# Kernel optimization log

Measured on AMD Instinct MI355X. Metric: run time of the kernel, lower is better.

The kernel has to match this reference:

```python
import jax, jax.numpy as jnp
from jax import lax
import numpy as np

EPS = 1e-12      # F.normalize eps
TOP_N = 250      # top negatives selected
SMOOTH = 1e-5    # soft dice smooth


def _dilate10(m):
    # == 10 iterations of 3x3x3 binary max-pool dilation. m: [B,D,H,W] float.
    for _ in range(10):
        m = lax.reduce_window(m, 0.0, lax.max, (1, 3, 3, 3), (1, 1, 1, 1), 'SAME')
    return m


def _self_loss(feature, lab):
    # feature: [B,C,D,H,W], lab: [B,D,H,W] int
    feat = jnp.moveaxis(feature, 1, -1)                       # [B,D,H,W,C]
    pos = (lab == 1)
    posf = pos.astype(feat.dtype)
    cnt = posf.sum()
    std = (feat * posf[..., None]).sum((0, 1, 2, 3)) / jnp.maximum(cnt, 1.0)
    std = jnp.where(cnt > 0, std, 0.0)                        # [C]
    std_n = std / jnp.maximum(jnp.linalg.norm(std), EPS)
    feat_n = feat / jnp.maximum(jnp.linalg.norm(feat, axis=-1, keepdims=True), EPS)
    # cosine similarity of per-voxel normalized features vs normalized mean positive
    sim = jnp.einsum('bdhwc,c->bdhw', feat_n, std_n)

    # positive term: mean over positives of (1 - sim)
    pos_loss = jnp.where(cnt > 0, ((1.0 - sim) * posf).sum() / jnp.maximum(cnt, 1.0), 0.0)

    # easily-misclassified ring: dilate(pos,10) & ~pos; mean relu(sim)
    mis = (_dilate10(posf) > 0) & (~pos)
    misf = mis.astype(sim.dtype)
    mcnt = misf.sum()
    mis_loss = jnp.where(mcnt > 0, (jax.nn.relu(sim) * misf).sum() / jnp.maximum(mcnt, 1.0), 0.0)

    # hard negatives: top-250 sims among label==0, scatter to mask, dilate, & ~pos
    neg = (lab == 0)
    neg_sims = jnp.where(neg, sim, -jnp.inf).reshape(-1)
    top_vals, top_idx = lax.top_k(neg_sims, TOP_N)
    hsm = jnp.zeros(neg_sims.shape[0], sim.dtype).at[top_idx].set(
        jnp.where(jnp.isfinite(top_vals), 1.0, 0.0)).reshape(sim.shape)
    fin = (_dilate10(hsm) > 0) & (~pos)
    finf = fin.astype(sim.dtype)
    fcnt = finf.sum()
    neg_loss = jnp.where(fcnt > 0, (jax.nn.relu(sim) * finf).sum() / jnp.maximum(fcnt, 1.0), 0.0)

    return pos_loss + mis_loss + neg_loss


def _ce_dice(net_output, target):
    lab = target[:, 0]                                        # [B,D,H,W]
    logp = jax.nn.log_softmax(net_output, axis=1)
    ce = -jnp.mean(jnp.take_along_axis(logp, target, axis=1))
    probs = jnp.exp(logp)                                     # softmax_helper_dim1
    nc = net_output.shape[1]
    onehot = jax.nn.one_hot(lab, nc, axis=1, dtype=probs.dtype)  # [B,nc,D,H,W]
    axes = (0, 2, 3, 4)                                       # batch_dice=True
    tp = (probs * onehot).sum(axes)
    fp = (probs * (1.0 - onehot)).sum(axes)
    fn = ((1.0 - probs) * onehot).sum(axes)
    dc = (2.0 * tp + SMOOTH) / (2.0 * tp + fp + fn + SMOOTH + 1e-8)
    dice = -jnp.mean(dc[1:])                                  # do_bg=False
    return ce, dice


def reference(feature, net_output, target):
    ce, dice = _ce_dice(net_output, target)
    sl = _self_loss(feature, target[:, 0])
    return 1.0 * ce + 1.0 * dice + 5.0 * sl


def setup_inputs():
    key = jax.random.key(0)
    k1, k2, k3 = jax.random.split(key, 3)
    B, C, D, H, W = 2, 32, 64, 128, 128
    NC = 2
    feature = jax.random.normal(k1, (B, C, D, H, W), jnp.float32)
    net_output = jax.random.normal(k2, (B, NC, D, H, W), jnp.float32)
    target = jax.random.randint(k3, (B, 1, D, H, W), 0, 2).astype(jnp.int32)
    return {'feature': feature, 'net_output': net_output, 'target': target}
```

## Files before the change

### kernel.cpp

```cpp
#include <hip/hip_runtime.h>
#include <stdint.h>

typedef unsigned int u32;
typedef unsigned long long u64;

#define BB 2
#define CC 32
#define DD 64
#define HH 128
#define WW 128
#define SS (DD*HH*WW)
#define NN (BB*SS)
#define NQ (NN/4)
#define NWORDS (NN/64)
#define EPSF 1e-12f
#define TOPN 250u

struct Ctrl {
  u32 done4, tie, pad0, pad1;
};

struct Acc {
  double ce, tp, fp, fn;
  double stdsum[CC];
  double pos_num, mis_num, fin_num;
  u64 cnt, mcnt, fcnt;
};

__device__ __forceinline__ float waveRedF(float v){
#pragma unroll
  for (int o = 32; o; o >>= 1) v += __shfl_xor(v, o);
  return v;
}
__device__ __forceinline__ u32 waveRedU(u32 v){
#pragma unroll
  for (int o = 32; o; o >>= 1) v += __shfl_xor(v, o);
  return v;
}
__device__ __forceinline__ void red_d(double* dst, float v, volatile float* sh){
  int lane = threadIdx.x & 63, wid = threadIdx.x >> 6;
  v = waveRedF(v);
  if (lane == 0) sh[wid] = v;
  __syncthreads();
  if (threadIdx.x == 0){
    float t = 0.f;
    for (int i = 0; i < (int)(blockDim.x >> 6); i++) t += sh[i];
    atomicAdd(dst, (double)t);
  }
  __syncthreads();
}
__device__ __forceinline__ void red_u(u64* dst, u32 v, volatile u32* sh){
  int lane = threadIdx.x & 63, wid = threadIdx.x >> 6;
  v = waveRedU(v);
  if (lane == 0) sh[wid] = v;
  __syncthreads();
  if (threadIdx.x == 0){
    u32 t = 0;
    for (int i = 0; i < (int)(blockDim.x >> 6); i++) t += sh[i];
    atomicAdd(dst, (u64)t);
  }
  __syncthreads();
}

__device__ __forceinline__ u32 sortkey(float f){
  u32 u = __float_as_uint(f);
  return (u & 0x80000000u) ? ~u : (u | 0x80000000u);
}

__device__ __forceinline__ void select_top(const u32* __restrict__ hist, u32 nbins,
                                           u32 k, u32* shres, u32* binOut, u32* kremOut){
  __syncthreads();
  if (threadIdx.x < 64){
    int lane = threadIdx.x;
    u32 running = 0; bool found = false;
    for (u32 chunk = 0; chunk * 64 < nbins && !found; chunk++){
      int bin = (int)nbins - 1 - (int)(chunk * 64 + (u32)lane);
      u32 val = (bin >= 0) ? hist[bin] : 0u;
      u32 p = val;
#pragma unroll
      for (int o = 1; o < 64; o <<= 1){ u32 t = __shfl_up(p, o); if (lane >= o) p += t; }
      u32 tot = __shfl(p, 63);
      u32 incl = running + p, excl = incl - val;
      bool hit = (excl < k) && (incl >= k);
      u64 mb = __ballot(hit);
      if (mb){
        int hl = __ffsll((unsigned long long)mb) - 1;
        if (lane == hl){ shres[0] = (u32)bin; shres[1] = k - excl; }
        found = true;
      } else running += tot;
    }
    if (!found && lane == 0){ shres[0] = 0; shres[1] = k; }
  }
  __syncthreads();
  *binOut = shres[0]; *kremOut = shres[1];
}

__global__ __launch_bounds__(256) void k_ce(const float* __restrict__ net,
                                            const int* __restrict__ tgt,
                                            u64* __restrict__ pbits, Acc* acc){
  __shared__ u32 nibsh[256];
  __shared__ float shf[4]; __shared__ u32 shu[4];
  float ce = 0.f, tp = 0.f, fp = 0.f, fnn = 0.f;
  u32 cnt = 0;
  const u32 stride = 1024u * 256u;
#pragma unroll 1
  for (u32 it = 0; it < 2; it++){
    u32 q = blockIdx.x * 256u + threadIdx.x + it * stride;
    u32 v = q * 4u;
    u32 b = v >> 20, s = v & (SS - 1);
    int4 l4 = *(const int4*)(tgt + v);
    u32 nib = (l4.x ? 1u : 0u) | (l4.y ? 2u : 0u) | (l4.z ? 4u : 0u) | (l4.w ? 8u : 0u);
    cnt += __popc(nib);
    __syncthreads();
    nibsh[threadIdx.x] = nib;
    {
      const float* nb = net + (size_t)(b * 2) * SS + s;
      float4 x0 = *(const float4*)(nb);
      float4 x1 = *(const float4*)(nb + SS);
      float xs0[4] = {x0.x, x0.y, x0.z, x0.w};
      float xs1[4] = {x1.x, x1.y, x1.z, x1.w};
#pragma unroll
      for (int j = 0; j < 4; j++){
        int lab = (nib >> j) & 1;
        float m = fmaxf(xs0[j], xs1[j]);
        float lse = m + logf(expf(xs0[j] - m) + expf(xs1[j] - m));
        ce += lse - (lab ? xs1[j] : xs0[j]);
        float p1 = expf(xs1[j] - lse);
        if (lab){ tp += p1; fnn += 1.0f - p1; } else fp += p1;
      }
    }
    __syncthreads();
    if (threadIdx.x < 16){
      u64 o = 0;
#pragma unroll
      for (int j = 0; j < 16; j++)
        o |= (u64)(nibsh[threadIdx.x * 16 + j] & 0xFu) << (4 * j);
      pbits[blockIdx.x * 16u + it * 16384u + threadIdx.x] = o;
    }
  }
  red_d(&acc->ce, ce, shf);
  red_d(&acc->tp, tp, shf);
  red_d(&acc->fp, fp, shf);
  red_d(&acc->fn, fnn, shf);
  red_u(&acc->cnt, cnt, shu);
}

__global__ __launch_bounds__(256) void k_std(const float* __restrict__ feat,
                                             const u64* __restrict__ pbits, Acc* acc){
  u32 c = blockIdx.x & 31u;
  u32 chunk = blockIdx.x >> 5;
  u32 vbase = chunk * 65536u;
  u32 b = vbase >> 20;
  u32 s0 = vbase & (SS - 1);
  const float* fp = feat + (size_t)b * CC * SS + (size_t)c * SS + s0;
  const u64* pb = pbits + (vbase >> 6);
  float a = 0.f;
#pragma unroll 8
  for (u32 i = 0; i < 64; i++){
    u32 off = i * 1024u + threadIdx.x * 4u;
    float4 f = *(const float4*)(fp + off);
    u32 bits = (u32)(pb[off >> 6] >> (off & 63u)) & 0xFu;
    if (bits & 1u) a += f.x;
    if (bits & 2u) a += f.y;
    if (bits & 4u) a += f.z;
    if (bits & 8u) a += f.w;
  }
  __shared__ float sh[4];
  int lane = threadIdx.x & 63, wid = threadIdx.x >> 6;
  a = waveRedF(a);
  if (lane == 0) sh[wid] = a;
  __syncthreads();
  if (threadIdx.x == 0)
    atomicAdd(&acc->stdsum[c], (double)(sh[0] + sh[1] + sh[2] + sh[3]));
}

__global__ __launch_bounds__(256) void k_sim(const float* __restrict__ feat,
                                             const u64* __restrict__ pbits,
                                             Acc* acc, float* __restrict__ sim,
                                             u32* __restrict__ h1){
  __shared__ float st[CC];
  __shared__ u32 lh[2048];
  __shared__ float shf[4];
  {
    u64 cnt = acc->cnt;
    float sv = 0.f;
    if (threadIdx.x < CC && cnt) sv = (float)(acc->stdsum[threadIdx.x] / (double)cnt);
    if (threadIdx.x < 64){
      float t = waveRedF(sv * sv);
      float d = fmaxf(sqrtf(t), EPSF);
      if (threadIdx.x < CC) st[threadIdx.x] = sv / d;
    }
  }
  for (u32 i = threadIdx.x; i < 2048u; i += 256u) lh[i] = 0;
  __syncthreads();
  u32 vbase = blockIdx.x * 4096u;
  u32 b = vbase >> 20;
  u32 s0 = vbase & (SS - 1);
  const float* fp = feat + (size_t)b * CC * SS + s0;
  float4 dt[4], n2[4];
#pragma unroll
  for (int g = 0; g < 4; g++){
    dt[g].x = dt[g].y = dt[g].z = dt[g].w = 0.f;
    n2[g].x = n2[g].y = n2[g].z = n2[g].w = 0.f;
  }
#pragma unroll 2
  for (u32 c = 0; c < CC; c++){
    float w = st[c];
    const float* fc = fp + (size_t)c * SS;
    float4 f[4];
#pragma unroll
    for (int g = 0; g < 4; g++)
      f[g] = *(const float4*)(fc + (u32)g * 1024u + threadIdx.x * 4u);
#pragma unroll
    for (int g = 0; g < 4; g++){
      dt[g].x += f[g].x * w; dt[g].y += f[g].y * w;
      dt[g].z += f[g].z * w; dt[g].w += f[g].w * w;
      n2[g].x += f[g].x * f[g].x; n2[g].y += f[g].y * f[g].y;
      n2[g].z += f[g].z * f[g].z; n2[g].w += f[g].w * f[g].w;
    }
  }
  float pn = 0.f;
#pragma unroll
  for (int g = 0; g < 4; g++){
    u32 off = (u32)g * 1024u + threadIdx.x * 4u;
    u32 v = vbase + off;
    float4 sm;
    sm.x = dt[g].x / fmaxf(sqrtf(n2[g].x), EPSF);
    sm.y = dt[g].y / fmaxf(sqrtf(n2[g].y), EPSF);
    sm.z = dt[g].z / fmaxf(sqrtf(n2[g].z), EPSF);
    sm.w = dt[g].w / fmaxf(sqrtf(n2[g].w), EPSF);
    *(float4*)(sim + v) = sm;
    u32 bits = (u32)(pbits[v >> 6] >> (v & 63u)) & 0xFu;
    float ss[4] = {sm.x, sm.y, sm.z, sm.w};
#pragma unroll
    for (int j = 0; j < 4; j++){
      if ((bits >> j) & 1u) pn += 1.f - ss[j];
      else atomicAdd(&lh[sortkey(ss[j]) >> 21], 1u);
    }
  }
  __syncthreads();
  for (u32 i = threadIdx.x; i < 2048u; i += 256u)
    if (lh[i]) atomicAdd(&h1[i], lh[i]);
  red_d(&acc->pos_num, pn, shf);
}

__device__ __forceinline__ void dilwh_slab(const u64* __restrict__ in, u64* __restrict__ out,
                                           u32 slab, u64* arr){
  u32 base = slab * 256u;
  int t = threadIdx.x;
  if (t < 128){
    u64 lo = in[base + 2 * t], hi = in[base + 2 * t + 1];
    u64 al = lo, ah = hi;
#pragma unroll
    for (int i = 0; i < 10; i++){ u64 c = al >> 63; ah = ah | (ah << 1) | c; al = al | (al << 1); }
    u64 bl = lo, bh = hi;
#pragma unroll
    for (int i = 0; i < 10; i++){ u64 c = bh << 63; bl = bl | (bl >> 1) | c; bh = bh | (bh >> 1); }
    arr[2 * t] = al | bl;
    arr[2 * t + 1] = ah | bh;
  }
  __syncthreads();
  int h = t >> 1, wj = t & 1;
  int h0 = h - 10 > 0 ? h - 10 : 0;
  int h1 = h + 10 < 127 ? h + 10 : 127;
  u64 o = 0;
  for (int hh = h0; hh <= h1; hh++) o |= arr[2 * hh + wj];
  out[base + (u32)t] = o;
  __syncthreads();
}

__global__ __launch_bounds__(256) void k_dilwh(const u64* __restrict__ in, u64* __restrict__ out){
  __shared__ u64 arr[256];
  dilwh_slab(in, out, blockIdx.x, arr);
}

__global__ __launch_bounds__(256) void k_histL2(const float* __restrict__ sim,
                                                const u64* __restrict__ pbits,
                                                const u32* __restrict__ h1,
                                                u32* __restrict__ h2,
                                                const u64* __restrict__ P,
                                                u64* __restrict__ T1P){
  __shared__ u64 arr[256];
  __shared__ u32 lh[2048];
  __shared__ u32 shres[2];
  if (blockIdx.x < 128u) dilwh_slab(P, T1P, blockIdx.x, arr);
  u32 p1, k1;
  select_top(h1, 2048, TOPN, shres, &p1, &k1);
  for (u32 i = threadIdx.x; i < 2048u; i += 256u) lh[i] = 0;
  __syncthreads();
  const u32 stride = 512u * 256u;
#pragma unroll 1
  for (u32 it = 0; it < 4; it++){
    u32 q = blockIdx.x * 256u + threadIdx.x + it * stride;
    u32 nib = (u32)(pbits[q >> 4] >> ((q & 15u) << 2)) & 0xFu;
    float4 s4 = *(const float4*)(sim + q * 4u);
    float ss[4] = {s4.x, s4.y, s4.z, s4.w};
#pragma unroll
    for (int j = 0; j < 4; j++){
      if (!((nib >> j) & 1u)){
        u32 key = sortkey(ss[j]);
        if ((key >> 21) == p1) atomicAdd(&lh[(key >> 10) & 2047u], 1u);
      }
    }
  }
  __syncthreads();
  for (u32 i = threadIdx.x; i < 2048u; i += 256u)
    if (lh[i]) atomicAdd(&h2[i], lh[i]);
}

__global__ __launch_bounds__(256) void k_mark(const float* __restrict__ sim,
                                              const u64* __restrict__ pbits,
                                              u64* __restrict__ hs,
                                              const u32* __restrict__ h1,
                                              const u32* __restrict__ h2,
                                              Ctrl* ctrl){
  __shared__ u32 shres[2];
  u32 p1, k1, b2, k2;
  select_top(h1, 2048, TOPN, shres, &p1, &k1);
  select_top(h2, 2048, k1, shres, &b2, &k2);
  u32 p12 = (p1 << 11) | b2;
  int lane = threadIdx.x & 63;
  const u32 stride = 1024u * 256u;
#pragma unroll 1
  for (u32 it = 0; it < 8; it++){
    u32 v = blockIdx.x * 256u + threadIdx.x + it * stride;
    u64 w = pbits[v >> 6];
    bool neg = !((w >> (v & 63u)) & 1ull);
    bool seed = false;
    if (neg){
      u32 pref = sortkey(sim[v]) >> 10;
      if (pref > p12) seed = true;
      else if (pref == p12){
        u32 old = atomicAdd(&ctrl->tie, 1u);
        if (old < k2) seed = true;
      }
    }
    u64 mb = __ballot(seed);
    if (lane == 0) hs[v >> 6] = mb;
  }
}

__global__ __launch_bounds__(256) void k_final(const float* __restrict__ sim,
                                               const u64* __restrict__ P,
                                               const u64* __restrict__ T1P,
                                               const u64* __restrict__ T1H,
                                               Acc* acc, Ctrl* ctrl, float* out){
  __shared__ float shf[4]; __shared__ u32 shu[4];
  __shared__ int amLast;
  u32 wi = blockIdx.x * 256u + threadIdx.x;
  u32 wj = wi & 1u;
  u32 row = wi >> 1;
  int h = (int)(row & 127u);
  int d = (int)((row >> 7) & 63u);
  u32 b = row >> 13;
  int d0 = d - 10 > 0 ? d - 10 : 0;
  int d1 = d + 10 < 63 ? d + 10 : 63;
  const u64* bp = T1P + ((size_t)(b << 13) + (u32)h) * 2 + wj;
  const u64* bh = T1H + ((size_t)(b << 13) + (u32)h) * 2 + wj;
  u64 dpw = 0, dhw = 0;
  for (int dd = d0; dd <= d1; dd++){
    dpw |= bp[(size_t)dd * 256];
    dhw |= bh[(size_t)dd * 256];
  }
  u64 pw = P[wi];
  u64 mis = dpw & ~pw;
  u64 fin = dhw & ~pw;
  float mn = 0.f, fnm = 0.f;
  u32 mc = (u32)__popcll(mis), fc = (u32)__popcll(fin);
  const float* sp = sim + (size_t)wi * 64u;
#pragma unroll 1
  for (int jj = 0; jj < 16; jj++){
    float4 s4 = *(const float4*)(sp + jj * 4);
    float ss[4] = {s4.x, s4.y, s4.z, s4.w};
#pragma unroll
    for (int j = 0; j < 4; j++){
      int bit = jj * 4 + j;
      float r = fmaxf(ss[j], 0.f);
      if ((mis >> bit) & 1ull) mn += r;
      if ((fin >> bit) & 1ull) fnm += r;
    }
  }
  red_d(&acc->mis_num, mn, shf);
  red_d(&acc->fin_num, fnm, shf);
  red_u(&acc->mcnt, mc, shu);
  red_u(&acc->fcnt, fc, shu);
  __threadfence();
  if (threadIdx.x == 0) amLast = (atomicAdd(&ctrl->done4, 1u) == gridDim.x - 1);
  __syncthreads();
  if (amLast && threadIdx.x == 0){
    double ce = acc->ce / (double)NN;
    double tp = acc->tp, fp = acc->fp, fn = acc->fn;
    double dc1 = (2.0 * tp + 1e-5) / (2.0 * tp + fp + fn + 1e-5 + 1e-8);
    u64 cnt = acc->cnt;
    double pos_loss = cnt ? (acc->pos_num / (double)cnt) : 0.0;
    u64 mcnt = atomicAdd(&acc->mcnt, 0ull);
    u64 fcnt = atomicAdd(&acc->fcnt, 0ull);
    double mis_loss = mcnt ? (atomicAdd(&acc->mis_num, 0.0) / (double)mcnt) : 0.0;
    double neg_loss = fcnt ? (atomicAdd(&acc->fin_num, 0.0) / (double)fcnt) : 0.0;
    out[0] = (float)(ce - dc1 + 5.0 * (pos_loss + mis_loss + neg_loss));
  }
}

extern "C" void kernel_launch(void* const* d_in, const int* in_sizes, int n_in,
                              void* d_out, int out_size, void* d_ws, size_t ws_size,
                              hipStream_t stream){
  (void)in_sizes; (void)n_in; (void)out_size; (void)ws_size;
  const float* feat = (const float*)d_in[0];
  const float* net  = (const float*)d_in[1];
  const int*   tgt  = (const int*)d_in[2];
  float* out = (float*)d_out;
  char* ws = (char*)d_ws;

  size_t off = 0;
  auto take = [&](size_t bytes) -> void* {
    void* p = (void*)(ws + off);
    off += (bytes + 255) & ~(size_t)255;
    return p;
  };
  float* sim = (float*)take((size_t)NN * 4);
  u64* P   = (u64*)take((size_t)NWORDS * 8);
  u64* T1P = (u64*)take((size_t)NWORDS * 8);
  u64* HS  = (u64*)take((size_t)NWORDS * 8);
  u64* T1H = (u64*)take((size_t)NWORDS * 8);
  size_t zstart = off;
  u32* h1 = (u32*)take(2048 * 4);
  u32* h2 = (u32*)take(2048 * 4);
  Ctrl* ctrl = (Ctrl*)take(sizeof(Ctrl));
  Acc* acc = (Acc*)take(sizeof(Acc));
  hipMemsetAsync(ws + zstart, 0, off - zstart, stream);

  k_ce<<<1024, 256, 0, stream>>>(net, tgt, P, acc);
  k_std<<<1024, 256, 0, stream>>>(feat, P, acc);
  k_sim<<<512, 256, 0, stream>>>(feat, P, acc, sim, h1);
  k_histL2<<<512, 256, 0, stream>>>(sim, P, h1, h2, P, T1P);
  k_mark<<<1024, 256, 0, stream>>>(sim, P, HS, h1, h2, ctrl);
  k_dilwh<<<128, 256, 0, stream>>>(HS, T1H);
  k_final<<<128, 256, 0, stream>>>(sim, P, T1P, T1H, acc, ctrl, out);
}
```

Baseline: 533.8 us.

## Split label bitpacking from CE; merge CE and std into one launch; drop memset

A new pre-pass packs the labels into the positive bitmask, writes per-block positive counts, and zeroes the accumulator region itself, which replaces the hipMemsetAsync call. The cross-entropy/dice accumulation and the per-channel positive-feature sums now run as two block ranges of a single kernel, so the big feature read overlaps the net_output read. k_sim reduces the per-block counts itself instead of reading an atomically accumulated count. This cuts one launch and the memset, and removes the count atomics. In exchange the labels are traversed once more as bits, and the CE blocks are few (64) and long-running.

```diff
diff --git a/kernel.cpp b/kernel.cpp
--- a/kernel.cpp
+++ b/kernel.cpp
@@ -95,25 +95,53 @@
   *binOut = shres[0]; *kremOut = shres[1];
 }
 
-__global__ __launch_bounds__(256) void k_ce(const float* __restrict__ net,
-                                            const int* __restrict__ tgt,
-                                            u64* __restrict__ pbits, Acc* acc){
+__global__ __launch_bounds__(256) void k_pre(const int* __restrict__ tgt,
+                                             u64* __restrict__ pbits,
+                                             u32* __restrict__ cntArr,
+                                             u32* __restrict__ zptr, u32 zwords){
   __shared__ u32 nibsh[256];
-  __shared__ float shf[4]; __shared__ u32 shu[4];
-  float ce = 0.f, tp = 0.f, fp = 0.f, fnn = 0.f;
+  __shared__ u32 shu[4];
+  if (blockIdx.x == 0){
+    for (u32 i = threadIdx.x; i < zwords; i += 256u) zptr[i] = 0;
+  }
   u32 cnt = 0;
-  const u32 stride = 1024u * 256u;
 #pragma unroll 1
-  for (u32 it = 0; it < 2; it++){
-    u32 q = blockIdx.x * 256u + threadIdx.x + it * stride;
-    u32 v = q * 4u;
-    u32 b = v >> 20, s = v & (SS - 1);
-    int4 l4 = *(const int4*)(tgt + v);
+  for (u32 it = 0; it < 4; it++){
+    u32 q = blockIdx.x * 1024u + it * 256u + threadIdx.x;
+    int4 l4 = *(const int4*)(tgt + q * 4u);
     u32 nib = (l4.x ? 1u : 0u) | (l4.y ? 2u : 0u) | (l4.z ? 4u : 0u) | (l4.w ? 8u : 0u);
     cnt += __popc(nib);
     __syncthreads();
     nibsh[threadIdx.x] = nib;
-    {
+    __syncthreads();
+    if (threadIdx.x < 16){
+      u64 o = 0;
+#pragma unroll
+      for (int j = 0; j < 16; j++)
+        o |= (u64)(nibsh[threadIdx.x * 16 + j] & 0xFu) << (4 * j);
+      pbits[blockIdx.x * 64u + it * 16u + threadIdx.x] = o;
+    }
+  }
+  int lane = threadIdx.x & 63, wid = threadIdx.x >> 6;
+  cnt = waveRedU(cnt);
+  if (lane == 0) shu[wid] = cnt;
+  __syncthreads();
+  if (threadIdx.x == 0) cntArr[blockIdx.x] = shu[0] + shu[1] + shu[2] + shu[3];
+}
+
+__global__ __launch_bounds__(256) void k_ce_std(const float* __restrict__ feat,
+                                                const float* __restrict__ net,
+                                                const u64* __restrict__ pbits, Acc* acc){
+  __shared__ float sh[16];
+  if (blockIdx.x < 64u){
+    u32 bid = blockIdx.x;
+    float ce = 0.f, tp = 0.f, fp = 0.f, fnn = 0.f;
+#pragma unroll 1
+    for (u32 it = 0; it < 32; it++){
+      u32 q = bid * 8192u + it * 256u + threadIdx.x;
+      u32 nib = (u32)(pbits[q >> 4] >> ((q & 15u) << 2)) & 0xFu;
+      u32 v = q * 4u;
+      u32 b = v >> 20, s = v & (SS - 1);
       const float* nb = net + (size_t)(b * 2) * SS + s;
       float4 x0 = *(const float4*)(nb);
       float4 x1 = *(const float4*)(nb + SS);
@@ -129,60 +157,65 @@
         if (lab){ tp += p1; fnn += 1.0f - p1; } else fp += p1;
       }
     }
+    int lane = threadIdx.x & 63, wid = threadIdx.x >> 6;
+    ce = waveRedF(ce); tp = waveRedF(tp); fp = waveRedF(fp); fnn = waveRedF(fnn);
+    if (lane == 0){ sh[wid] = ce; sh[4 + wid] = tp; sh[8 + wid] = fp; sh[12 + wid] = fnn; }
     __syncthreads();
-    if (threadIdx.x < 16){
-      u64 o = 0;
-#pragma unroll
-      for (int j = 0; j < 16; j++)
-        o |= (u64)(nibsh[threadIdx.x * 16 + j] & 0xFu) << (4 * j);
-      pbits[blockIdx.x * 16u + it * 16384u + threadIdx.x] = o;
-    }
-  }
-  red_d(&acc->ce, ce, shf);
-  red_d(&acc->tp, tp, shf);
-  red_d(&acc->fp, fp, shf);
-  red_d(&acc->fn, fnn, shf);
-  red_u(&acc->cnt, cnt, shu);
-}
-
-__global__ __launch_bounds__(256) void k_std(const float* __restrict__ feat,
-                                             const u64* __restrict__ pbits, Acc* acc){
-  u32 c = blockIdx.x & 31u;
-  u32 chunk = blockIdx.x >> 5;
-  u32 vbase = chunk * 65536u;
-  u32 b = vbase >> 20;
-  u32 s0 = vbase & (SS - 1);
-  const float* fp = feat + (size_t)b * CC * SS + (size_t)c * SS + s0;
-  const u64* pb = pbits + (vbase >> 6);
-  float a = 0.f;
+    if (threadIdx.x == 0){
+      atomicAdd(&acc->ce, (double)(sh[0] + sh[1] + sh[2] + sh[3]));
+      atomicAdd(&acc->tp, (double)(sh[4] + sh[5] + sh[6] + sh[7]));
+      atomicAdd(&acc->fp, (double)(sh[8] + sh[9] + sh[10] + sh[11]));
+      atomicAdd(&acc->fn, (double)(sh[12] + sh[13] + sh[14] + sh[15]));
+    }
+  } else {
+    u32 bx = blockIdx.x - 64u;
+    u32 c = bx & 31u;
+    u32 chunk = bx >> 5;
+    u32 vbase = chunk * 65536u;
+    u32 b = vbase >> 20;
+    u32 s0 = vbase & (SS - 1);
+    const float* fp_ = feat + (size_t)b * CC * SS + (size_t)c * SS + s0;
+    const u64* pb = pbits + (vbase >> 6);
+    float a = 0.f;
 #pragma unroll 8
-  for (u32 i = 0; i < 64; i++){
-    u32 off = i * 1024u + threadIdx.x * 4u;
-    float4 f = *(const float4*)(fp + off);
-    u32 bits = (u32)(pb[off >> 6] >> (off & 63u)) & 0xFu;
-    if (bits & 1u) a += f.x;
-    if (bits & 2u) a += f.y;
-    if (bits & 4u) a += f.z;
-    if (bits & 8u) a += f.w;
-  }
-  __shared__ float sh[4];
-  int lane = threadIdx.x & 63, wid = threadIdx.x >> 6;
-  a = waveRedF(a);
-  if (lane == 0) sh[wid] = a;
-  __syncthreads();
-  if (threadIdx.x == 0)
-    atomicAdd(&acc->stdsum[c], (double)(sh[0] + sh[1] + sh[2] + sh[3]));
+    for (u32 i = 0; i < 64; i++){
+      u32 off = i * 1024u + threadIdx.x * 4u;
+      float4 f = *(const float4*)(fp_ + off);
+      u32 bits = (u32)(pb[off >> 6] >> (off & 63u)) & 0xFu;
+      if (bits & 1u) a += f.x;
+      if (bits & 2u) a += f.y;
+      if (bits & 4u) a += f.z;
+      if (bits & 8u) a += f.w;
+    }
+    int lane = threadIdx.x & 63, wid = threadIdx.x >> 6;
+    a = waveRedF(a);
+    if (lane == 0) sh[wid] = a;
+    __syncthreads();
+    if (threadIdx.x == 0)
+      atomicAdd(&acc->stdsum[c], (double)(sh[0] + sh[1] + sh[2] + sh[3]));
+  }
 }
 
 __global__ __launch_bounds__(256) void k_sim(const float* __restrict__ feat,
                                              const u64* __restrict__ pbits,
+                                             const u32* __restrict__ cntArr,
                                              Acc* acc, float* __restrict__ sim,
                                              u32* __restrict__ h1){
   __shared__ float st[CC];
   __shared__ u32 lh[2048];
   __shared__ float shf[4];
+  __shared__ u32 scnt;
+  if (threadIdx.x < 64){
+    u32 sc = 0;
+#pragma unroll
+    for (int i = 0; i < 8; i++) sc += cntArr[threadIdx.x * 8 + i];
+    sc = waveRedU(sc);
+    if (threadIdx.x == 0) scnt = sc;
+  }
+  __syncthreads();
+  u32 cnt = scnt;
+  if (blockIdx.x == 0 && threadIdx.x == 0) acc->cnt = (u64)cnt;
   {
-    u64 cnt = acc->cnt;
     float sv = 0.f;
     if (threadIdx.x < CC && cnt) sv = (float)(acc->stdsum[threadIdx.x] / (double)cnt);
     if (threadIdx.x < 64){
@@ -422,16 +455,17 @@
   u64* T1P = (u64*)take((size_t)NWORDS * 8);
   u64* HS  = (u64*)take((size_t)NWORDS * 8);
   u64* T1H = (u64*)take((size_t)NWORDS * 8);
+  u32* cntArr = (u32*)take(512 * 4);
   size_t zstart = off;
   u32* h1 = (u32*)take(2048 * 4);
   u32* h2 = (u32*)take(2048 * 4);
   Ctrl* ctrl = (Ctrl*)take(sizeof(Ctrl));
   Acc* acc = (Acc*)take(sizeof(Acc));
-  hipMemsetAsync(ws + zstart, 0, off - zstart, stream);
-
-  k_ce<<<1024, 256, 0, stream>>>(net, tgt, P, acc);
-  k_std<<<1024, 256, 0, stream>>>(feat, P, acc);
-  k_sim<<<512, 256, 0, stream>>>(feat, P, acc, sim, h1);
+  u32 zwords = (u32)((off - zstart) >> 2);
+
+  k_pre<<<512, 256, 0, stream>>>(tgt, P, cntArr, (u32*)(ws + zstart), zwords);
+  k_ce_std<<<1088, 256, 0, stream>>>(feat, net, P, acc);
+  k_sim<<<512, 256, 0, stream>>>(feat, P, cntArr, acc, sim, h1);
   k_histL2<<<512, 256, 0, stream>>>(sim, P, h1, h2, P, T1P);
   k_mark<<<1024, 256, 0, stream>>>(sim, P, HS, h1, h2, ctrl);
   k_dilwh<<<128, 256, 0, stream>>>(HS, T1H);
```

New measurement: 487.1 us. 1.1x faster.
